# Optimization experiments

Hardware: AMD Instinct MI355X
Metric: run time of the kernel (lower is better)

Reference implementation:

```python
import jax, jax.numpy as jnp
import numpy as np

NUM_CLASSES = 80
NUM_KERNELS = 256
NUM_GRIDS = (40, 36, 24, 16, 12)
STRIDES = (8, 8, 16, 32, 32)
SCORE_THR = 0.1
MASK_THR = 0.5
UPDATE_THR = 0.05
NMS_PRE = 500
MAX_PER_IMG = 100
NMS_SIGMA = 2.0
ORI_H, ORI_W = 640, 960  # ratio*f_h = 4*160, 4*240 -> upsampled == ori size


def point_nms(heat, kernel=2):
    # torch: hmax = max_pool2d(heat, 2, stride=1, padding=1)[..., :-1, :-1]
    # equivalent: 2x2 window with (1,0) padding top/left, -inf init
    hmax = jax.lax.reduce_window(
        heat, -jnp.inf, jax.lax.max,
        (1, 1, kernel, kernel), (1, 1, 1, 1),
        ((0, 0), (0, 0), (1, 0), (1, 0)))
    return heat * (hmax == heat).astype(heat.dtype)


def setup_inputs() -> dict:
    key = jax.random.key(0)
    ks = jax.random.split(key, 11)
    inp = {}
    for i, g in enumerate(NUM_GRIDS):
        inp[f"cate_p{i}"] = jax.random.normal(ks[i], (1, NUM_CLASSES, g, g), jnp.float32)
        inp[f"kern_p{i}"] = jax.random.normal(ks[5 + i], (1, NUM_KERNELS, g, g), jnp.float32) * 0.05
    inp["mask_feat"] = jax.random.normal(ks[10], (1, NUM_KERNELS, 160, 240), jnp.float32)
    return inp


def _solo_post(cate_list, kern_list, mask_feat):
    # point-NMS on sigmoid scores, flatten grids, concat levels  -> [S, C]
    cate = jnp.concatenate([
        point_nms(jax.nn.sigmoid(c))[0].transpose(1, 2, 0).reshape(-1, NUM_CLASSES)
        for c in cate_list], axis=0)
    kern = jnp.concatenate([
        k[0].transpose(1, 2, 0).reshape(-1, NUM_KERNELS) for k in kern_list], axis=0)
    strides = jnp.concatenate([
        jnp.full((g * g,), float(s), jnp.float32) for g, s in zip(NUM_GRIDS, STRIDES)])

    # score threshold -> fixed-size top-k selection (jit-friendly)
    flat = jnp.where(cate > SCORE_THR, cate, 0.0).reshape(-1)  # [S*C]
    scores, flat_idx = jax.lax.top_k(flat, NMS_PRE)
    grid_idx = flat_idx // NUM_CLASSES
    labels = flat_idx % NUM_CLASSES
    valid = scores > 0.0

    # 1x1 dynamic conv == matmul over channel dim
    kp = kern[grid_idx]                                   # [N, K]
    st = strides[grid_idx]                                # [N]
    seg = jax.nn.sigmoid(jnp.einsum('nk,khw->nhw', kp, mask_feat[0]))  # [N, h, w]
    seg_masks = seg > MASK_THR
    sum_masks = seg_masks.sum((1, 2)).astype(jnp.float32)
    keep = (sum_masks > st) & valid
    seg_score = (seg * seg_masks).sum((1, 2)) / jnp.maximum(sum_masks, 1.0)
    scores = scores * seg_score * keep.astype(scores.dtype)

    # sort descending by updated scores
    order = jnp.argsort(-scores)
    scores = scores[order]
    labels = labels[order]
    seg = seg[order]
    alive = (scores > 0.0).astype(jnp.float32)
    masks_f = seg_masks[order].astype(jnp.float32) * alive[:, None, None]
    sum_m = masks_f.sum((1, 2))

    # matrix NMS (gaussian)
    mflat = masks_f.reshape(NMS_PRE, -1)
    inter = mflat @ mflat.T                               # [N, N]
    union = sum_m[:, None] + sum_m[None, :] - inter
    iou = jnp.triu(jnp.where(union > 0, inter / jnp.maximum(union, 1.0), 0.0), k=1)
    label_m = jnp.triu((labels[:, None] == labels[None, :]).astype(jnp.float32), k=1)
    decay_iou = iou * label_m
    comp_iou = decay_iou.max(axis=0)                      # per instance (column max)
    # decay[i, j] = exp(-sigma*(decay_iou[i,j]^2 - comp_iou[i]^2)); coef = min over i
    decay = jnp.exp(-NMS_SIGMA * (decay_iou ** 2 - comp_iou[:, None] ** 2))
    scores = scores * decay.min(axis=0)

    scores = scores * (scores >= UPDATE_THR).astype(scores.dtype)
    top_s, top_i = jax.lax.top_k(scores, MAX_PER_IMG)
    seg_top = seg[top_i]                                  # [M, h, w]

    # upsample to (f_h*ratio, f_w*ratio) then to ori_size (equal here), crop no-op
    up = jax.image.resize(seg_top, (MAX_PER_IMG, ORI_H, ORI_W), method='bilinear')
    up2 = jax.image.resize(up, (MAX_PER_IMG, ORI_H, ORI_W), method='bilinear')
    return up2, top_s, top_i, labels


def reference(cate_p0, cate_p1, cate_p2, cate_p3, cate_p4,
              kern_p0, kern_p1, kern_p2, kern_p3, kern_p4, mask_feat):
    up2, top_s, top_i, labels = _solo_post(
        [cate_p0, cate_p1, cate_p2, cate_p3, cate_p4],
        [kern_p0, kern_p1, kern_p2, kern_p3, kern_p4], mask_feat)
    pred_masks = up2 > MASK_THR
    return pred_masks, top_s, labels[top_i]
```

## Files before the change

kernel.cpp:

```cpp
#include <hip/hip_runtime.h>
#include <stdint.h>

#define NCLS 80
#define NKER 256
#define STOT 3872
#define NFLAT (STOT*NCLS)
#define NPRE 500
#define NPREP 512
#define MAXI 100
#define MH 160
#define MW 240
#define MP (MH*MW)
#define OH 640
#define OW 960
#define NWORD 600
#define PARTW 300
#define UCAP 32768
#define TAU 5e-4f

#define BN 128
#define BP 128
#define BK 16

#define WS_HIST   0u
#define WS_META   262144u
#define WS_CMP    266240u
#define WS_CORR   270336u
#define WS_ZEROB  274432u
#define WS_PIOU   274432u
#define WS_CANDV  1272432u
#define WS_CANDI  1288816u
#define WS_FLAT   2266240u
#define WS_KP     2790528u
#define WS_SEL    3538048u
#define WS_KPT    3591296u
#define WS_MB     4115584u
#define WS_PART   6515584u
#define WS_SEG    7715584u
#define WS_ULIST  46115584u
#define WS_UZ     46246656u
#define WS_PLIST  WS_FLAT

__device__ __forceinline__ float bf2f(unsigned short u) { return __uint_as_float(((unsigned)u) << 16); }
__device__ __forceinline__ unsigned short f2bf(float f) {
  unsigned b = __float_as_uint(f);
  return (unsigned short)((b + 0x7fffu + ((b >> 16) & 1u)) >> 16);
}
__device__ __forceinline__ unsigned fkey(float f) {
  unsigned b = __float_as_uint(f);
  return b ^ ((b & 0x80000000u) ? 0xFFFFFFFFu : 0x80000000u);
}

__global__ __launch_bounds__(256) void k_flat(
    const float* __restrict__ c0, const float* __restrict__ c1, const float* __restrict__ c2,
    const float* __restrict__ c3, const float* __restrict__ c4,
    float* __restrict__ flat, unsigned* __restrict__ hist) {
  int idx = blockIdx.x * 256 + threadIdx.x;
  if (idx >= NFLAT) return;
  int s = idx / NCLS, c = idx - s * NCLS;
  const float* base; int g, cell;
  if (s < 1600)      { base = c0; g = 40; cell = s; }
  else if (s < 2896) { base = c1; g = 36; cell = s - 1600; }
  else if (s < 3472) { base = c2; g = 24; cell = s - 2896; }
  else if (s < 3728) { base = c3; g = 16; cell = s - 3472; }
  else               { base = c4; g = 12; cell = s - 3728; }
  int i = cell / g, j = cell - i * g;
  const float* ch = base + c * g * g;
  float x = ch[i * g + j];
  float m = x;
  if (i > 0 && j > 0) m = fmaxf(m, ch[(i - 1) * g + j - 1]);
  if (i > 0)          m = fmaxf(m, ch[(i - 1) * g + j]);
  if (j > 0)          m = fmaxf(m, ch[i * g + j - 1]);
  bool pass = (x >= m) && ((double)x > -2.1972245773362196 );
  flat[idx] = pass ? x : __int_as_float(0xFF800000);
  if (pass) atomicAdd(&hist[fkey(x) >> 16], 1u);
}

__global__ void k_pivot(const unsigned* __restrict__ hist, unsigned* __restrict__ meta) {
  __shared__ unsigned csum[1024];
  int t = threadIdx.x;
  int hi = 65536 - t * 64, lo = hi - 64;
  unsigned s = 0;
  for (int b = lo; b < hi; ++b) s += hist[b];
  csum[t] = s;
  __syncthreads();
  if (t == 0) {
    unsigned cum = 0;
    for (int cch = 0; cch < 1024; ++cch) {
      if (cum + csum[cch] >= NPRE) {
        int chi = 65536 - cch * 64;
        for (int b = chi - 1; b >= chi - 64; --b) {
          if (cum + hist[b] >= NPRE) { meta[1] = (unsigned)b; return; }
          cum += hist[b];
        }
      }
      cum += csum[cch];
    }
    meta[1] = 0u;
  }
}

__global__ __launch_bounds__(256) void k_compact(
    const float* __restrict__ flat, float* __restrict__ cv, int* __restrict__ ci,
    unsigned* __restrict__ meta) {
  int idx = blockIdx.x * 256 + threadIdx.x;
  if (idx >= NFLAT) return;
  float v = flat[idx];
  if (__float_as_uint(v) == 0xFF800000u) return;
  if ((fkey(v) >> 16) >= meta[1]) {
    unsigned pos = atomicAdd(&meta[0], 1u);
    if (pos < 4096u) { cv[pos] = v; ci[pos] = idx; }
  }
}

__global__ __launch_bounds__(1024) void k_select(
    const float* __restrict__ cv, const int* __restrict__ ci, const unsigned* __restrict__ meta,
    double* __restrict__ sel_score, unsigned* __restrict__ sel_grid,
    unsigned* __restrict__ sel_label, double* __restrict__ sel_stride) {
  __shared__ float sv[4096];
  __shared__ int si[4096];
  int t = threadIdx.x;
  int n = (meta[0] < 4096u) ? (int)meta[0] : 4096;
  for (int i = t; i < 4096; i += 1024) {
    if (i < n) { sv[i] = cv[i]; si[i] = ci[i]; }
    else       { sv[i] = __int_as_float(0xFF800000); si[i] = (1 << 30) + i; }
  }
  __syncthreads();
  for (int k = 2; k <= 4096; k <<= 1)
    for (int j = k >> 1; j > 0; j >>= 1) {
      for (int i = t; i < 4096; i += 1024) {
        int ix = i ^ j;
        if (ix > i) {
          float v1 = sv[i], v2 = sv[ix]; int i1 = si[i], i2 = si[ix];
          bool b2 = (v2 > v1) || (v2 == v1 && i2 < i1);
          bool dir = (i & k) == 0;
          if (dir == b2) { sv[i] = v2; sv[ix] = v1; si[i] = i2; si[ix] = i1; }
        }
      }
      __syncthreads();
    }
  for (int i = t; i < NPREP; i += 1024) {
    if (i < NPRE && i < n) {
      int fidx = si[i];
      unsigned gi = (unsigned)fidx / NCLS;
      sel_score[i] = 1.0 / (1.0 + exp(-(double)sv[i]));
      sel_grid[i] = gi;
      sel_label[i] = (unsigned)fidx - gi * NCLS;
      sel_stride[i] = gi < 2896u ? 8.0 : (gi < 3472u ? 16.0 : 32.0);
    } else {
      sel_score[i] = 0.0; sel_grid[i] = 0u; sel_label[i] = 0u; sel_stride[i] = 1e18;
    }
  }
}

__global__ __launch_bounds__(256) void k_gather(
    const float* __restrict__ k0, const float* __restrict__ k1, const float* __restrict__ k2,
    const float* __restrict__ k3, const float* __restrict__ k4,
    const unsigned* __restrict__ sel_grid, float* __restrict__ kpT, float* __restrict__ kp) {
  int tid = blockIdx.x * 256 + threadIdx.x;
  if (tid >= NPREP * NKER) return;
  int n = tid & (NPREP - 1);
  int k = tid >> 9;
  float v = 0.f;
  if (n < NPRE) {
    unsigned gi = sel_grid[n];
    const float* base; unsigned g, cell;
    if (gi < 1600u)      { base = k0; g = 40; cell = gi; }
    else if (gi < 2896u) { base = k1; g = 36; cell = gi - 1600u; }
    else if (gi < 3472u) { base = k2; g = 24; cell = gi - 2896u; }
    else if (gi < 3728u) { base = k3; g = 16; cell = gi - 3472u; }
    else                 { base = k4; g = 12; cell = gi - 3728u; }
    v = base[(unsigned)k * g * g + cell];
  }
  kpT[k * NPREP + n] = v;
  kp[n * NKER + k] = v;
}

__global__ __launch_bounds__(256, 4) void k_gemm(
    const float* __restrict__ kpT, const float* __restrict__ mf,
    unsigned short* __restrict__ seg, unsigned long long* __restrict__ mb,
    double* __restrict__ part, unsigned* __restrict__ ulist, float* __restrict__ uz,
    unsigned* __restrict__ meta) {
  __shared__ float Asf[BK][BN];
  __shared__ float Bsf[BK][BP];
  int p0 = blockIdx.x * BP, n0 = blockIdx.y * BN;
  int tid = threadIdx.x;
  int tp = tid & 15, tn = tid >> 4;
  float acc[8][8] = {};
  float2 ra[4], rb[4];
#pragma unroll
  for (int it = 0; it < 4; ++it) {
    int q = it * 256 + tid; int row = q >> 6, c2 = q & 63;
    ra[it] = *(const float2*)&kpT[row * NPREP + n0 + c2 * 2];
    rb[it] = *(const float2*)&mf[(size_t)row * MP + p0 + c2 * 2];
  }
  for (int kc = 0; kc < NKER; kc += BK) {
#pragma unroll
    for (int it = 0; it < 4; ++it) {
      int q = it * 256 + tid; int row = q >> 6, c2 = q & 63;
      *(float2*)&Asf[row][c2 * 2] = ra[it];
      *(float2*)&Bsf[row][c2 * 2] = rb[it];
    }
    __syncthreads();
    if (kc + BK < NKER) {
#pragma unroll
      for (int it = 0; it < 4; ++it) {
        int q = it * 256 + tid; int row = q >> 6, c2 = q & 63;
        ra[it] = *(const float2*)&kpT[(kc + BK + row) * NPREP + n0 + c2 * 2];
        rb[it] = *(const float2*)&mf[(size_t)(kc + BK + row) * MP + p0 + c2 * 2];
      }
    }
#pragma unroll 4
    for (int k = 0; k < BK; ++k) {
      float4 A0 = *(float4*)&Asf[k][tn * 8 + 0];
      float4 A1 = *(float4*)&Asf[k][tn * 8 + 4];
      float4 B0 = *(float4*)&Bsf[k][tp * 4];
      float4 B1 = *(float4*)&Bsf[k][64 + tp * 4];
      float a[8] = {A0.x, A0.y, A0.z, A0.w, A1.x, A1.y, A1.z, A1.w};
      float b[8] = {B0.x, B0.y, B0.z, B0.w, B1.x, B1.y, B1.z, B1.w};
#pragma unroll
      for (int r = 0; r < 8; ++r)
#pragma unroll
        for (int c = 0; c < 8; ++c)
          acc[r][c] = fmaf(a[r], b[c], acc[r][c]);
    }
    __syncthreads();
  }
  double* partL = (double*)&Asf[0][0];
  __shared__ unsigned nibL[128][16];
#pragma unroll
  for (int r = 0; r < 8; ++r) {
    int nl = (tn << 3) + r;
    int nn = n0 + nl;
    unsigned nb = 0; double wsum = 0.0;
    unsigned short u[8];
#pragma unroll
    for (int c = 0; c < 8; ++c) {
      float z = acc[r][c];
      float sf = 1.0f / (1.0f + __expf(-z));
      u[c] = f2bf(sf);
      if (z > 0.0f) { nb |= 1u << c; wsum += (double)sf; }
    }
    if (nn < NPRE) {
#pragma unroll
      for (int c = 0; c < 8; ++c) {
        float z = acc[r][c];
        if (fabsf(z) < TAU) {
          unsigned pos = atomicAdd(&meta[3], 1u);
          if (pos < UCAP) {
            int p = p0 + (c >> 2) * 64 + tp * 4 + (c & 3);
            ulist[pos] = ((unsigned)nn << 16) | (unsigned)p;
            uz[pos] = z;
          }
        }
      }
#pragma unroll
      for (int g = 0; g < 2; ++g) {
        ushort4 o; o.x = u[4 * g]; o.y = u[4 * g + 1]; o.z = u[4 * g + 2]; o.w = u[4 * g + 3];
        *(ushort4*)&seg[(size_t)nn * MP + p0 + g * 64 + tp * 4] = o;
      }
    }
    partL[nl * 16 + tp] = wsum;
    nibL[nl][tp] = nb;
  }
  __syncthreads();
  if (tid < 128) {
    int nn = n0 + tid;
    if (nn < NPRE) {
      double ssum = 0.0; unsigned long long w0 = 0ull, w1 = 0ull;
#pragma unroll
      for (int c = 0; c < 16; ++c) {
        ssum += partL[tid * 16 + c];
        unsigned long long nb = (unsigned long long)nibL[tid][c];
        w0 |= (nb & 0xFull) << (c * 4);
        w1 |= ((nb >> 4) & 0xFull) << (c * 4);
      }
      int bx = blockIdx.x;
      part[nn * PARTW + bx] = ssum;
      mb[nn * NWORD + bx * 2] = w0;
      mb[nn * NWORD + bx * 2 + 1] = w1;
    }
  }
}

__global__ __launch_bounds__(256) void k_patch(
    const float* __restrict__ kp, const float* __restrict__ mf,
    const unsigned* __restrict__ ulist, const float* __restrict__ uz,
    const unsigned* __restrict__ meta,
    unsigned long long* __restrict__ mb, double* __restrict__ corr) {
  unsigned cnt = meta[3]; if (cnt > UCAP) cnt = UCAP;
  int wid = (blockIdx.x * 256 + threadIdx.x) >> 6;
  int lane = threadIdx.x & 63;
  for (unsigned e = wid; e < cnt; e += 256) {
    unsigned pk = ulist[e];
    int n = (int)(pk >> 16), p = (int)(pk & 0xFFFFu);
    double d = 0.0;
#pragma unroll
    for (int i = 0; i < 4; ++i) {
      int k = lane + 64 * i;
      d = fma((double)kp[n * NKER + k], (double)mf[(size_t)k * MP + p], d);
    }
    for (int o = 32; o > 0; o >>= 1) d += __shfl_down(d, o);
    if (lane == 0) {
      float z32 = uz[e];
      bool b32 = z32 > 0.0f;
      bool b64 = d > 0.0;
      if (b32 != b64) {
        atomicXor(&mb[(size_t)n * NWORD + (p >> 6)], 1ull << (p & 63));
        float sf = 1.0f / (1.0f + __expf(-z32));
        atomicAdd(&corr[n], b64 ? (double)sf : -(double)sf);
      }
    }
  }
}

__global__ void k_masks(const unsigned long long* __restrict__ mb, const double* __restrict__ part,
                        const double* __restrict__ corr,
                        const double* __restrict__ sel_score, const double* __restrict__ sel_stride,
                        double* __restrict__ summask, double* __restrict__ upd) {
  int n = blockIdx.x, t = threadIdx.x;
  int cnt = 0; double ws = 0.0;
  for (int j = t; j < NWORD; j += 64) cnt += __popcll(mb[n * NWORD + j]);
  for (int j = t; j < PARTW; j += 64) ws += part[n * PARTW + j];
  for (int o = 32; o > 0; o >>= 1) { cnt += __shfl_down(cnt, o); ws += __shfl_down(ws, o); }
  if (t == 0) {
    ws += corr[n];
    double cf = (double)cnt;
    double ss = ws / fmax(cf, 1.0);
    double raw = sel_score[n];
    bool keep = (cf > sel_stride[n]) && (raw > 0.0);
    summask[n] = cf;
    upd[n] = keep ? raw * ss : 0.0;
  }
}

__global__ __launch_bounds__(512) void k_sort(
    const double* __restrict__ upd, const unsigned* __restrict__ sel_label, const double* __restrict__ summask,
    double* __restrict__ s_score, unsigned* __restrict__ s_slot, unsigned* __restrict__ s_label2,
    double* __restrict__ s_sum, unsigned* __restrict__ plist, unsigned* __restrict__ meta) {
  __shared__ double sv[NPREP];
  __shared__ int si[NPREP];
  __shared__ unsigned labv[NPREP];
  int t = threadIdx.x;
  sv[t] = (t < NPRE) ? upd[t] : -1.0;
  si[t] = t;
  __syncthreads();
  for (int k = 2; k <= NPREP; k <<= 1)
    for (int j = k >> 1; j > 0; j >>= 1) {
      int ix = t ^ j;
      if (ix > t) {
        double v1 = sv[t], v2 = sv[ix]; int i1 = si[t], i2 = si[ix];
        bool b2 = (v2 > v1) || (v2 == v1 && i2 < i1);
        bool dir = (t & k) == 0;
        if (dir == b2) { sv[t] = v2; sv[ix] = v1; si[t] = i2; si[ix] = i1; }
      }
      __syncthreads();
    }
  double sc = sv[t]; int slot = si[t];
  bool alive = sc > 0.0;
  unsigned lab = sel_label[slot];
  s_score[t] = alive ? sc : 0.0;
  s_slot[t] = (unsigned)slot;
  s_label2[t] = lab;
  s_sum[t] = (alive && slot < NPRE) ? summask[slot] : 0.0;
  labv[t] = alive ? lab : (0x10000u + (unsigned)t);
  __syncthreads();
  if (t < NPRE) {
    unsigned li = labv[t];
    if (li < 0x10000u) {
      for (int j = t + 1; j < NPRE; ++j) {
        if (labv[j] == li) {
          unsigned pos = atomicAdd(&meta[2], 1u);
          plist[pos] = ((unsigned)t << 16) | (unsigned)j;
        }
      }
    }
  }
}

__global__ __launch_bounds__(256) void k_inter(
    const unsigned long long* __restrict__ mb, const unsigned* __restrict__ s_slot,
    const double* __restrict__ s_sum, const unsigned* __restrict__ plist,
    const unsigned* __restrict__ meta, double* __restrict__ piou,
    unsigned long long* __restrict__ cmp_bits) {
  int wid = (blockIdx.x * 256 + threadIdx.x) >> 6;
  int lane = threadIdx.x & 63;
  unsigned npair = meta[2];
  for (unsigned pp = wid; pp < npair; pp += 256) {
    unsigned pk = plist[pp];
    int i = (int)(pk >> 16), j = (int)(pk & 0xFFFFu);
    const unsigned long long* A = mb + (size_t)s_slot[i] * NWORD;
    const unsigned long long* B = mb + (size_t)s_slot[j] * NWORD;
    int c = 0;
    for (int wd = lane; wd < NWORD; wd += 64) c += __popcll(A[wd] & B[wd]);
    for (int o = 32; o > 0; o >>= 1) c += __shfl_down(c, o);
    if (lane == 0) {
      double inter = (double)c;
      double uni = s_sum[i] + s_sum[j] - inter;
      double val = (uni > 0.0) ? inter / fmax(uni, 1.0) : 0.0;
      piou[pp] = val;
      if (val > 0.0)
        atomicMax(&cmp_bits[j], (unsigned long long)__double_as_longlong(val));
    }
  }
}

__global__ __launch_bounds__(512) void k_top(
    const unsigned* __restrict__ plist, const unsigned* __restrict__ meta,
    const double* __restrict__ piou, const unsigned long long* __restrict__ cmp_bits,
    const double* __restrict__ s_score, const unsigned* __restrict__ s_label2,
    const unsigned* __restrict__ s_slot,
    float* __restrict__ d_out, int maskN, unsigned* __restrict__ up_slot) {
  __shared__ unsigned long long mS[NPREP];
  __shared__ double sv[NPREP];
  __shared__ int si[NPREP];
  int t = threadIdx.x;
  mS[t] = 0ull;
  __syncthreads();
  unsigned npair = meta[2];
  for (unsigned p = t; p < npair; p += NPREP) {
    unsigned pk = plist[p];
    int i = (int)(pk >> 16), j = (int)(pk & 0xFFFFu);
    double d = piou[p];
    double ci = __longlong_as_double((long long)cmp_bits[i]);
    double v = d * d - ci * ci;
    if (v > 0.0)
      atomicMax(&mS[j], (unsigned long long)__double_as_longlong(v));
  }
  __syncthreads();
  double f = 0.0;
  if (t < NPRE) {
    double m = __longlong_as_double((long long)mS[t]);
    f = s_score[t] * exp(-2.0 * m);
    if (f < 0.05) f = 0.0;
  }
  sv[t] = f; si[t] = t;
  __syncthreads();
  for (int k = 2; k <= NPREP; k <<= 1)
    for (int j = k >> 1; j > 0; j >>= 1) {
      int ix = t ^ j;
      if (ix > t) {
        double v1 = sv[t], v2 = sv[ix]; int i1 = si[t], i2 = si[ix];
        bool b2 = (v2 > v1) || (v2 == v1 && i2 < i1);
        bool dir = (t & k) == 0;
        if (dir == b2) { sv[t] = v2; sv[ix] = v1; si[t] = i2; si[ix] = i1; }
      }
      __syncthreads();
    }
  if (t < MAXI) {
    int pos = si[t];
    d_out[maskN + t] = (float)sv[t];
    d_out[maskN + MAXI + t] = (float)s_label2[pos];
    up_slot[t] = s_slot[pos];
  }
}

__global__ __launch_bounds__(256) void k_up(const unsigned short* __restrict__ seg,
                                            const unsigned* __restrict__ up_slot,
                                            float* __restrict__ out, int maskN) {
  int o4 = (blockIdx.x * 256 + threadIdx.x) * 4;
  if (o4 >= maskN) return;
  int m = o4 / (OH * OW);
  int rem = o4 - m * (OH * OW);
  int y = rem / OW;
  int x = rem - y * OW;
  int a = x >> 2;
  const unsigned short* row = seg + (size_t)up_slot[m] * MP;
  float sy = y * 0.25f - 0.375f;
  int y0 = (int)floorf(sy);
  float wy = sy - y0;
  int y0c = max(y0, 0), y1c = min(y0 + 1, MH - 1);
  const unsigned short* r0 = row + y0c * MW;
  const unsigned short* r1 = row + y1c * MW;
  int t0 = max(a - 1, 0), t1 = a, t2 = min(a + 1, MW - 1);
  float T0 = bf2f(r0[t0]), T1 = bf2f(r0[t1]), T2 = bf2f(r0[t2]);
  float B0 = bf2f(r1[t0]), B1 = bf2f(r1[t1]), B2 = bf2f(r1[t2]);
  float iwy = 1.f - wy;
  float4 o;
  o.x = iwy * (0.375f * T0 + 0.625f * T1) + wy * (0.375f * B0 + 0.625f * B1);
  o.y = iwy * (0.125f * T0 + 0.875f * T1) + wy * (0.125f * B0 + 0.875f * B1);
  o.z = iwy * (0.875f * T1 + 0.125f * T2) + wy * (0.875f * B1 + 0.125f * B2);
  o.w = iwy * (0.625f * T1 + 0.375f * T2) + wy * (0.625f * B1 + 0.375f * B2);
  o.x = (o.x > 0.5f) ? 1.f : 0.f;
  o.y = (o.y > 0.5f) ? 1.f : 0.f;
  o.z = (o.z > 0.5f) ? 1.f : 0.f;
  o.w = (o.w > 0.5f) ? 1.f : 0.f;
  *(float4*)&out[o4] = o;
}

extern "C" void kernel_launch(void* const* d_in, const int* in_sizes, int n_in,
                              void* d_out, int out_size, void* d_ws, size_t ws_size,
                              hipStream_t stream) {
  const float* c0 = (const float*)d_in[0];
  const float* k0 = (const float*)d_in[1];
  const float* c1 = (const float*)d_in[2];
  const float* k1 = (const float*)d_in[3];
  const float* c2 = (const float*)d_in[4];
  const float* k2 = (const float*)d_in[5];
  const float* c3 = (const float*)d_in[6];
  const float* k3 = (const float*)d_in[7];
  const float* c4 = (const float*)d_in[8];
  const float* k4 = (const float*)d_in[9];
  const float* mf = (const float*)d_in[10];

  char* ws = (char*)d_ws;
  unsigned* hist = (unsigned*)(ws + WS_HIST);
  unsigned* meta = (unsigned*)(ws + WS_META);
  unsigned long long* cmp_bits = (unsigned long long*)(ws + WS_CMP);
  double* corr = (double*)(ws + WS_CORR);
  double* piou = (double*)(ws + WS_PIOU);
  float* cv = (float*)(ws + WS_CANDV);
  int* ci = (int*)(ws + WS_CANDI);
  float* flat = (float*)(ws + WS_FLAT);
  float* kp = (float*)(ws + WS_KP);
  double* sel_score  = (double*)(ws + WS_SEL + 0);
  unsigned* sel_grid = (unsigned*)(ws + WS_SEL + 4096);
  unsigned* sel_label= (unsigned*)(ws + WS_SEL + 8192);
  double* sel_stride = (double*)(ws + WS_SEL + 12288);
  double* upd        = (double*)(ws + WS_SEL + 16384);
  double* summask    = (double*)(ws + WS_SEL + 20480);
  double* s_score    = (double*)(ws + WS_SEL + 24576);
  unsigned* s_slot   = (unsigned*)(ws + WS_SEL + 28672);
  unsigned* s_label2 = (unsigned*)(ws + WS_SEL + 32768);
  double* s_sum      = (double*)(ws + WS_SEL + 36864);
  unsigned* up_slot  = (unsigned*)(ws + WS_SEL + 49152);
  float* kpT = (float*)(ws + WS_KPT);
  unsigned long long* mb = (unsigned long long*)(ws + WS_MB);
  double* part = (double*)(ws + WS_PART);
  unsigned short* seg = (unsigned short*)(ws + WS_SEG);
  unsigned* plist = (unsigned*)(ws + WS_PLIST);
  unsigned* ulist = (unsigned*)(ws + WS_ULIST);
  float* uzp = (float*)(ws + WS_UZ);

  int maskN = out_size - 2 * MAXI;

  hipMemsetAsync(ws, 0, WS_ZEROB, stream);

  k_flat<<<(NFLAT + 255) / 256, 256, 0, stream>>>(c0, c1, c2, c3, c4, flat, hist);
  k_pivot<<<1, 1024, 0, stream>>>(hist, meta);
  k_compact<<<(NFLAT + 255) / 256, 256, 0, stream>>>(flat, cv, ci, meta);
  k_select<<<1, 1024, 0, stream>>>(cv, ci, meta, sel_score, sel_grid, sel_label, sel_stride);
  k_gather<<<(NPREP * NKER + 255) / 256, 256, 0, stream>>>(k0, k1, k2, k3, k4, sel_grid, kpT, kp);
  dim3 g6(MP / BP, NPREP / BN);
  k_gemm<<<g6, 256, 0, stream>>>(kpT, mf, seg, mb, part, ulist, uzp, meta);
  k_patch<<<64, 256, 0, stream>>>(kp, mf, ulist, uzp, meta, mb, corr);
  k_masks<<<NPRE, 64, 0, stream>>>(mb, part, corr, sel_score, sel_stride, summask, upd);
  k_sort<<<1, NPREP, 0, stream>>>(upd, sel_label, summask, s_score, s_slot, s_label2, s_sum, plist, meta);
  k_inter<<<64, 256, 0, stream>>>(mb, s_slot, s_sum, plist, meta, piou, cmp_bits);
  k_top<<<1, NPREP, 0, stream>>>(plist, meta, piou, cmp_bits, s_score, s_label2, s_slot,
                                 (float*)d_out, maskN, up_slot);
  k_up<<<(maskN / 4 + 255) / 256, 256, 0, stream>>>(seg, up_slot, (float*)d_out, maskN);
}
```

Baseline: 625.1 us.

## Use split-bf16 MFMA for mask GEMM and transposed features for patch dot products

Replaces the FP32 FMA tile GEMM with a three-term split-bf16 (hi/lo) MFMA GEMM, which approximates FP32 accuracy on the matrix cores. Mask bits and partial sums are now built with wave ballots and shuffle reductions. The uncertainty threshold and patch-list capacity are raised to absorb the extra error, and an optional transposed copy of mask_feat is written so the FP64 patch kernel can do coalesced dot products. The risks are more patch entries to correct, an extra transpose pass over the feature map, and scalar bf16 stores into shared memory with possible bank conflicts.

Result: slower. 754.7 us (+20.7%).

```diff
diff --git a/kernel.cpp b/kernel.cpp
--- a/kernel.cpp
+++ b/kernel.cpp
@@ -15,12 +15,8 @@
 #define OW 960
 #define NWORD 600
 #define PARTW 300
-#define UCAP 32768
-#define TAU 5e-4f
-
-#define BN 128
-#define BP 128
-#define BK 16
+#define UCAP 131072
+#define TAU 1e-3f
 
 #define WS_HIST   0u
 #define WS_META   262144u
@@ -33,13 +29,16 @@
 #define WS_FLAT   2266240u
 #define WS_KP     2790528u
 #define WS_SEL    3538048u
-#define WS_KPT    3591296u
 #define WS_MB     4115584u
 #define WS_PART   6515584u
 #define WS_SEG    7715584u
 #define WS_ULIST  46115584u
-#define WS_UZ     46246656u
+#define WS_UZ     46639872u
+#define WS_MFT    47164160u
 #define WS_PLIST  WS_FLAT
+
+typedef float f32x4 __attribute__((ext_vector_type(4)));
+typedef __bf16 bf16x8 __attribute__((ext_vector_type(8)));
 
 __device__ __forceinline__ float bf2f(unsigned short u) { return __uint_as_float(((unsigned)u) << 16); }
 __device__ __forceinline__ unsigned short f2bf(float f) {
@@ -156,7 +155,7 @@
 __global__ __launch_bounds__(256) void k_gather(
     const float* __restrict__ k0, const float* __restrict__ k1, const float* __restrict__ k2,
     const float* __restrict__ k3, const float* __restrict__ k4,
-    const unsigned* __restrict__ sel_grid, float* __restrict__ kpT, float* __restrict__ kp) {
+    const unsigned* __restrict__ sel_grid, float* __restrict__ kp) {
   int tid = blockIdx.x * 256 + threadIdx.x;
   if (tid >= NPREP * NKER) return;
   int n = tid & (NPREP - 1);
@@ -172,118 +171,171 @@
     else                 { base = k4; g = 12; cell = gi - 3728u; }
     v = base[(unsigned)k * g * g + cell];
   }
-  kpT[k * NPREP + n] = v;
   kp[n * NKER + k] = v;
 }
 
-__global__ __launch_bounds__(256, 4) void k_gemm(
-    const float* __restrict__ kpT, const float* __restrict__ mf,
+__global__ __launch_bounds__(256) void k_mft(const float* __restrict__ mf, float* __restrict__ mfT) {
+  __shared__ float t[32][33];
+  int p0 = blockIdx.x * 32, k0 = blockIdx.y * 32;
+  int tx = threadIdx.x & 31, ty = (threadIdx.x >> 5) * 4;
+#pragma unroll
+  for (int j = 0; j < 4; ++j)
+    t[ty + j][tx] = mf[(size_t)(k0 + ty + j) * MP + p0 + tx];
+  __syncthreads();
+#pragma unroll
+  for (int j = 0; j < 4; ++j)
+    mfT[(size_t)(p0 + ty + j) * NKER + k0 + tx] = t[tx][ty + j];
+}
+
+__global__ __launch_bounds__(256, 2) void k_gemm(
+    const float* __restrict__ kp, const float* __restrict__ mf,
     unsigned short* __restrict__ seg, unsigned long long* __restrict__ mb,
     double* __restrict__ part, unsigned* __restrict__ ulist, float* __restrict__ uz,
     unsigned* __restrict__ meta) {
-  __shared__ float Asf[BK][BN];
-  __shared__ float Bsf[BK][BP];
-  int p0 = blockIdx.x * BP, n0 = blockIdx.y * BN;
+  __shared__ unsigned short AhL[128][40], AlL[128][40];
+  __shared__ unsigned short BhL[128][40], BlL[128][40];
+  __shared__ unsigned short bits16[128][8];
+  __shared__ double wsumL[128][8];
+  int p0 = blockIdx.x * 128, n0 = blockIdx.y * 128;
   int tid = threadIdx.x;
-  int tp = tid & 15, tn = tid >> 4;
-  float acc[8][8] = {};
-  float2 ra[4], rb[4];
-#pragma unroll
-  for (int it = 0; it < 4; ++it) {
-    int q = it * 256 + tid; int row = q >> 6, c2 = q & 63;
-    ra[it] = *(const float2*)&kpT[row * NPREP + n0 + c2 * 2];
-    rb[it] = *(const float2*)&mf[(size_t)row * MP + p0 + c2 * 2];
-  }
-  for (int kc = 0; kc < NKER; kc += BK) {
+  int lane = tid & 63, w = tid >> 6;
+  int wn = w >> 1, wp = w & 1;
+  int lg = lane >> 4, ll = lane & 15;
+  f32x4 acc[4][4] = {};
+  for (int kc = 0; kc < NKER; kc += 32) {
 #pragma unroll
     for (int it = 0; it < 4; ++it) {
-      int q = it * 256 + tid; int row = q >> 6, c2 = q & 63;
-      *(float2*)&Asf[row][c2 * 2] = ra[it];
-      *(float2*)&Bsf[row][c2 * 2] = rb[it];
+      int f4 = it * 256 + tid;
+      int n = f4 >> 3, kk = (f4 & 7) * 4;
+      float4 v = *(const float4*)&kp[(size_t)(n0 + n) * NKER + kc + kk];
+      unsigned short h0 = f2bf(v.x), h1 = f2bf(v.y), h2 = f2bf(v.z), h3 = f2bf(v.w);
+      ushort4 hv; hv.x = h0; hv.y = h1; hv.z = h2; hv.w = h3;
+      ushort4 lv; lv.x = f2bf(v.x - bf2f(h0)); lv.y = f2bf(v.y - bf2f(h1));
+      lv.z = f2bf(v.z - bf2f(h2)); lv.w = f2bf(v.w - bf2f(h3));
+      *(ushort4*)&AhL[n][kk] = hv;
+      *(ushort4*)&AlL[n][kk] = lv;
+    }
+#pragma unroll
+    for (int it = 0; it < 4; ++it) {
+      int f4 = it * 256 + tid;
+      int k = f4 >> 5, pp = (f4 & 31) * 4;
+      float4 v = *(const float4*)&mf[(size_t)(kc + k) * MP + p0 + pp];
+      float vv[4] = {v.x, v.y, v.z, v.w};
+#pragma unroll
+      for (int j = 0; j < 4; ++j) {
+        unsigned short h = f2bf(vv[j]);
+        BhL[pp + j][k] = h;
+        BlL[pp + j][k] = f2bf(vv[j] - bf2f(h));
+      }
     }
     __syncthreads();
-    if (kc + BK < NKER) {
-#pragma unroll
-      for (int it = 0; it < 4; ++it) {
-        int q = it * 256 + tid; int row = q >> 6, c2 = q & 63;
-        ra[it] = *(const float2*)&kpT[(kc + BK + row) * NPREP + n0 + c2 * 2];
-        rb[it] = *(const float2*)&mf[(size_t)(kc + BK + row) * MP + p0 + c2 * 2];
-      }
-    }
-#pragma unroll 4
-    for (int k = 0; k < BK; ++k) {
-      float4 A0 = *(float4*)&Asf[k][tn * 8 + 0];
-      float4 A1 = *(float4*)&Asf[k][tn * 8 + 4];
-      float4 B0 = *(float4*)&Bsf[k][tp * 4];
-      float4 B1 = *(float4*)&Bsf[k][64 + tp * 4];
-      float a[8] = {A0.x, A0.y, A0.z, A0.w, A1.x, A1.y, A1.z, A1.w};
-      float b[8] = {B0.x, B0.y, B0.z, B0.w, B1.x, B1.y, B1.z, B1.w};
-#pragma unroll
-      for (int r = 0; r < 8; ++r)
-#pragma unroll
-        for (int c = 0; c < 8; ++c)
-          acc[r][c] = fmaf(a[r], b[c], acc[r][c]);
+    bf16x8 ah[4], al[4];
+#pragma unroll
+    for (int tN = 0; tN < 4; ++tN) {
+      int nr = wn * 64 + tN * 16 + ll;
+      ah[tN] = *(const bf16x8*)&AhL[nr][lg * 8];
+      al[tN] = *(const bf16x8*)&AlL[nr][lg * 8];
+    }
+#pragma unroll
+    for (int tP = 0; tP < 4; ++tP) {
+      int pr = wp * 64 + tP * 16 + ll;
+      bf16x8 bh = *(const bf16x8*)&BhL[pr][lg * 8];
+      bf16x8 bl = *(const bf16x8*)&BlL[pr][lg * 8];
+#pragma unroll
+      for (int tN = 0; tN < 4; ++tN) {
+        acc[tN][tP] = __builtin_amdgcn_mfma_f32_16x16x32_bf16(al[tN], bh, acc[tN][tP], 0, 0, 0);
+        acc[tN][tP] = __builtin_amdgcn_mfma_f32_16x16x32_bf16(ah[tN], bl, acc[tN][tP], 0, 0, 0);
+        acc[tN][tP] = __builtin_amdgcn_mfma_f32_16x16x32_bf16(ah[tN], bh, acc[tN][tP], 0, 0, 0);
+      }
     }
     __syncthreads();
   }
-  double* partL = (double*)&Asf[0][0];
-  __shared__ unsigned nibL[128][16];
-#pragma unroll
-  for (int r = 0; r < 8; ++r) {
-    int nl = (tn << 3) + r;
-    int nn = n0 + nl;
-    unsigned nb = 0; double wsum = 0.0;
-    unsigned short u[8];
-#pragma unroll
-    for (int c = 0; c < 8; ++c) {
-      float z = acc[r][c];
-      float sf = 1.0f / (1.0f + __expf(-z));
-      u[c] = f2bf(sf);
-      if (z > 0.0f) { nb |= 1u << c; wsum += (double)sf; }
-    }
-    if (nn < NPRE) {
-#pragma unroll
-      for (int c = 0; c < 8; ++c) {
-        float z = acc[r][c];
-        if (fabsf(z) < TAU) {
-          unsigned pos = atomicAdd(&meta[3], 1u);
-          if (pos < UCAP) {
-            int p = p0 + (c >> 2) * 64 + tp * 4 + (c & 3);
-            ulist[pos] = ((unsigned)nn << 16) | (unsigned)p;
-            uz[pos] = z;
+#pragma unroll
+  for (int tN = 0; tN < 4; ++tN) {
+#pragma unroll
+    for (int tP = 0; tP < 4; ++tP) {
+#pragma unroll
+      for (int r = 0; r < 4; ++r) {
+        float z = acc[tN][tP][r];
+        bool pos = z > 0.0f;
+        unsigned long long bal = __ballot(pos);
+        int nloc = wn * 64 + tN * 16 + lg * 4 + r;
+        int nn = n0 + nloc;
+        float sf = 1.0f / (1.0f + __expf(-z));
+        if (nn < NPRE) {
+          seg[(size_t)nn * MP + p0 + wp * 64 + tP * 16 + ll] = f2bf(sf);
+          if (fabsf(z) < TAU) {
+            unsigned q = atomicAdd(&meta[3], 1u);
+            if (q < UCAP) {
+              int p = p0 + wp * 64 + tP * 16 + ll;
+              ulist[q] = ((unsigned)nn << 16) | (unsigned)p;
+              uz[q] = z;
+            }
           }
         }
-      }
-#pragma unroll
-      for (int g = 0; g < 2; ++g) {
-        ushort4 o; o.x = u[4 * g]; o.y = u[4 * g + 1]; o.z = u[4 * g + 2]; o.w = u[4 * g + 3];
-        *(ushort4*)&seg[(size_t)nn * MP + p0 + g * 64 + tp * 4] = o;
-      }
-    }
-    partL[nl * 16 + tp] = wsum;
-    nibL[nl][tp] = nb;
+        double v = pos ? (double)sf : 0.0;
+        v += __shfl_xor(v, 1); v += __shfl_xor(v, 2);
+        v += __shfl_xor(v, 4); v += __shfl_xor(v, 8);
+        if (ll == 0) {
+          bits16[nloc][wp * 4 + tP] = (unsigned short)((bal >> (lg * 16)) & 0xFFFFull);
+          wsumL[nloc][wp * 4 + tP] = v;
+        }
+      }
+    }
   }
   __syncthreads();
   if (tid < 128) {
     int nn = n0 + tid;
     if (nn < NPRE) {
-      double ssum = 0.0; unsigned long long w0 = 0ull, w1 = 0ull;
-#pragma unroll
-      for (int c = 0; c < 16; ++c) {
-        ssum += partL[tid * 16 + c];
-        unsigned long long nb = (unsigned long long)nibL[tid][c];
-        w0 |= (nb & 0xFull) << (c * 4);
-        w1 |= ((nb >> 4) & 0xFull) << (c * 4);
+      unsigned long long w0 = 0ull, w1 = 0ull;
+      double s = 0.0;
+#pragma unroll
+      for (int tP = 0; tP < 4; ++tP) {
+        w0 |= ((unsigned long long)bits16[tid][tP]) << (tP * 16);
+        w1 |= ((unsigned long long)bits16[tid][4 + tP]) << (tP * 16);
+        s += wsumL[tid][tP] + wsumL[tid][4 + tP];
       }
       int bx = blockIdx.x;
-      part[nn * PARTW + bx] = ssum;
-      mb[nn * NWORD + bx * 2] = w0;
-      mb[nn * NWORD + bx * 2 + 1] = w1;
-    }
-  }
-}
-
-__global__ __launch_bounds__(256) void k_patch(
+      mb[(size_t)nn * NWORD + bx * 2] = w0;
+      mb[(size_t)nn * NWORD + bx * 2 + 1] = w1;
+      part[nn * PARTW + bx] = s;
+    }
+  }
+}
+
+__global__ __launch_bounds__(256) void k_patch_t(
+    const float* __restrict__ kp, const float* __restrict__ mfT,
+    const unsigned* __restrict__ ulist, const float* __restrict__ uz,
+    const unsigned* __restrict__ meta,
+    unsigned long long* __restrict__ mb, double* __restrict__ corr) {
+  unsigned cnt = meta[3]; if (cnt > UCAP) cnt = UCAP;
+  int wid = (blockIdx.x * 256 + threadIdx.x) >> 6;
+  int lane = threadIdx.x & 63;
+  for (unsigned e = wid; e < cnt; e += 256) {
+    unsigned pk = ulist[e];
+    int n = (int)(pk >> 16), p = (int)(pk & 0xFFFFu);
+    float4 a = *(const float4*)&kp[(size_t)n * NKER + lane * 4];
+    float4 b = *(const float4*)&mfT[(size_t)p * NKER + lane * 4];
+    double d = 0.0;
+    d = fma((double)a.x, (double)b.x, d);
+    d = fma((double)a.y, (double)b.y, d);
+    d = fma((double)a.z, (double)b.z, d);
+    d = fma((double)a.w, (double)b.w, d);
+    for (int o = 32; o > 0; o >>= 1) d += __shfl_down(d, o);
+    if (lane == 0) {
+      float z32 = uz[e];
+      bool b32 = z32 > 0.0f;
+      bool b64 = d > 0.0;
+      if (b32 != b64) {
+        atomicXor(&mb[(size_t)n * NWORD + (p >> 6)], 1ull << (p & 63));
+        float sf = 1.0f / (1.0f + __expf(-z32));
+        atomicAdd(&corr[n], b64 ? (double)sf : -(double)sf);
+      }
+    }
+  }
+}
+
+__global__ __launch_bounds__(256) void k_patch_s(
     const float* __restrict__ kp, const float* __restrict__ mf,
     const unsigned* __restrict__ ulist, const float* __restrict__ uz,
     const unsigned* __restrict__ meta,
@@ -524,15 +576,16 @@
   unsigned* s_label2 = (unsigned*)(ws + WS_SEL + 32768);
   double* s_sum      = (double*)(ws + WS_SEL + 36864);
   unsigned* up_slot  = (unsigned*)(ws + WS_SEL + 49152);
-  float* kpT = (float*)(ws + WS_KPT);
   unsigned long long* mb = (unsigned long long*)(ws + WS_MB);
   double* part = (double*)(ws + WS_PART);
   unsigned short* seg = (unsigned short*)(ws + WS_SEG);
   unsigned* plist = (unsigned*)(ws + WS_PLIST);
   unsigned* ulist = (unsigned*)(ws + WS_ULIST);
   float* uzp = (float*)(ws + WS_UZ);
+  float* mfT = (float*)(ws + WS_MFT);
 
   int maskN = out_size - 2 * MAXI;
+  bool use_mft = ws_size >= (size_t)WS_MFT + (size_t)MP * NKER * 4;
 
   hipMemsetAsync(ws, 0, WS_ZEROB, stream);
 
@@ -540,10 +593,15 @@
   k_pivot<<<1, 1024, 0, stream>>>(hist, meta);
   k_compact<<<(NFLAT + 255) / 256, 256, 0, stream>>>(flat, cv, ci, meta);
   k_select<<<1, 1024, 0, stream>>>(cv, ci, meta, sel_score, sel_grid, sel_label, sel_stride);
-  k_gather<<<(NPREP * NKER + 255) / 256, 256, 0, stream>>>(k0, k1, k2, k3, k4, sel_grid, kpT, kp);
-  dim3 g6(MP / BP, NPREP / BN);
-  k_gemm<<<g6, 256, 0, stream>>>(kpT, mf, seg, mb, part, ulist, uzp, meta);
-  k_patch<<<64, 256, 0, stream>>>(kp, mf, ulist, uzp, meta, mb, corr);
+  k_gather<<<(NPREP * NKER + 255) / 256, 256, 0, stream>>>(k0, k1, k2, k3, k4, sel_grid, kp);
+  if (use_mft)
+    k_mft<<<dim3(MP / 32, NKER / 32), 256, 0, stream>>>(mf, mfT);
+  dim3 g6(MP / 128, NPREP / 128);
+  k_gemm<<<g6, 256, 0, stream>>>(kp, mf, seg, mb, part, ulist, uzp, meta);
+  if (use_mft)
+    k_patch_t<<<64, 256, 0, stream>>>(kp, mfT, ulist, uzp, meta, mb, corr);
+  else
+    k_patch_s<<<64, 256, 0, stream>>>(kp, mf, ulist, uzp, meta, mb, corr);
   k_masks<<<NPRE, 64, 0, stream>>>(mb, part, corr, sel_score, sel_stride, summask, upd);
   k_sort<<<1, NPREP, 0, stream>>>(upd, sel_label, summask, s_score, s_slot, s_label2, s_sum, plist, meta);
   k_inter<<<64, 256, 0, stream>>>(mb, s_slot, s_sum, plist, meta, piou, cmp_bits);
```
